# Kernel optimization log

Hardware: AMD Instinct MI355X
Metric: run time of the kernel (lower is better)

Reference implementation:

```python
import jax, jax.numpy as jnp
import numpy as np

NEG_INF = -10000.0


def setup_inputs() -> dict:
    key = jax.random.key(0)
    k_feats, k_mask, k_trans = jax.random.split(key, 3)
    B, S, T = 512, 1024, 64
    feats = jax.random.normal(k_feats, (B, S, T), dtype=jnp.float32)
    masks = jnp.ones((B, S), dtype=jnp.float32)
    # transitions: randn with row 0 and column 0 forced to -10000 (as in __init__)
    transitions = jax.random.normal(k_trans, (T, T), dtype=jnp.float32)
    transitions = transitions.at[:, 0].set(NEG_INF)
    transitions = transitions.at[0, :].set(NEG_INF)
    return {"feats": feats, "masks": masks, "transitions": transitions}


def reference(feats, masks, transitions):
    # feats: [B, S, T], masks: [B, S] float, transitions: [T_next? , T] -> scores
    # scores[b, j, k] = alpha[b, k] + transitions[j, k] + feats[b, i, j]
    # alpha_new[b, j] = logsumexp_k scores[b, j, k]
    alpha0 = feats[:, 0]                      # [B, T]
    feats_t = jnp.swapaxes(feats[:, 1:], 0, 1)   # [S-1, B, T]
    masks_t = masks[:, 1:].T                     # [S-1, B]

    def step(alpha, xm):
        feat_i, mask_i = xm                      # [B, T], [B]
        scores = alpha[:, None, :] + transitions[None] + feat_i[:, :, None]
        new_alpha = jax.scipy.special.logsumexp(scores, axis=2)  # [B, T]
        m = mask_i[:, None]
        alpha = new_alpha * m + alpha * (1.0 - m)
        return alpha, None

    alpha, _ = jax.lax.scan(step, alpha0, (feats_t, masks_t))
    return alpha
```

## Files before the change

kernel.cpp:

```cpp
#include <hip/hip_runtime.h>


typedef _Float16 __attribute__((ext_vector_type(2))) half2v;
typedef _Float16 __attribute__((ext_vector_type(8))) half8v;

constexpr int T    = 64;
constexpr int D    = 6;
constexpr int SMAX = 1024;

__device__ __forceinline__ float fdot2(half2v a, half2v b, float c) {
#if __has_builtin(__builtin_amdgcn_fdot2)
    return __builtin_amdgcn_fdot2(a, b, c, false);
#else
    return fmaf((float)a[0], (float)b[0], fmaf((float)a[1], (float)b[1], c));
#endif
}

__global__ __launch_bounds__(64, 1)
void crf_fwd_kernel(const float* __restrict__ feats,
                    const float* __restrict__ masks,
                    const float* __restrict__ trans,
                    float* __restrict__ out, int S)
{
    const int lane = threadIdx.x;
    const int b    = blockIdx.x;

    __shared__ __attribute__((aligned(16))) _Float16 sh[T];
    __shared__ float shm[SMAX];

    const float* mb = masks + (size_t)b * S;
    for (int w = lane; w < S; w += T) shm[w] = mb[w];

    const float* tr = trans + lane * T;
    float rmax = tr[0];
    for (int j = 1; j < T; ++j) rmax = fmaxf(rmax, tr[j]);
    half2v E[32];
#pragma unroll
    for (int k = 0; k < 32; ++k) {
        E[k][0] = (_Float16)__expf(tr[2 * k]     - rmax);
        E[k][1] = (_Float16)__expf(tr[2 * k + 1] - rmax);
    }

    __syncthreads();

    const float* fb = feats + (size_t)b * S * T;

    const float f0 = fb[lane];
    float u  = __expf(f0);
    _Float16 uh = (_Float16)u;
    float cacc = 0.f;
    float hsnap = 1.f, csnap = 0.f, Rsnap = 0.f, fsnap = f0;

    float f[D], mk[D];
#pragma unroll
    for (int k = 0; k < D; ++k) {
        f[k]  = fb[(size_t)(1 + k) * T + lane];
        mk[k] = shm[1 + k];
    }

#define CRF_STEP(FV, MV)                                                      \
    {                                                                         \
        const float ef = __expf((FV) + rmax);                  \
        const bool  mm = (MV) > 0.5f;                                         \
        __builtin_amdgcn_wave_barrier();                                      \
        sh[lane] = uh;                                                        \
        __builtin_amdgcn_wave_barrier();                                      \
        union { half8v v; half2v h2[4]; } blk[8];                             \
        _Pragma("unroll")                                                     \
        for (int r = 0; r < 8; ++r)                                           \
            blk[r].v = *(const half8v*)(sh + 8 * r);       \
        __builtin_amdgcn_wave_barrier();                                      \
        float ac0 = 0.f, ac1 = 0.f, ac2 = 0.f, ac3 = 0.f;                     \
        float ac4 = 0.f, ac5 = 0.f, ac6 = 0.f, ac7 = 0.f;                     \
        _Pragma("unroll")                                                     \
        for (int r = 0; r < 8; r += 2) {                                      \
            ac0 = fdot2(E[4 * r + 0], blk[r].h2[0], ac0);                     \
            ac1 = fdot2(E[4 * r + 1], blk[r].h2[1], ac1);                     \
            ac2 = fdot2(E[4 * r + 2], blk[r].h2[2], ac2);                     \
            ac3 = fdot2(E[4 * r + 3], blk[r].h2[3], ac3);                     \
            ac4 = fdot2(E[4 * r + 4], blk[r + 1].h2[0], ac4);                 \
            ac5 = fdot2(E[4 * r + 5], blk[r + 1].h2[1], ac5);                 \
            ac6 = fdot2(E[4 * r + 6], blk[r + 1].h2[2], ac6);                 \
            ac7 = fdot2(E[4 * r + 7], blk[r + 1].h2[3], ac7);                 \
        }                                                                     \
        const float total = ((ac0 + ac1) + (ac2 + ac3))                       \
                          + ((ac4 + ac5) + (ac6 + ac7));                      \
                         \
        const int hb = __builtin_amdgcn_readlane(__float_as_int(total), 0);   \
        const int e  = ((hb >> 23) & 255) - 127;                              \
        const float un = ldexpf(ef * total, -e);                              \
        hsnap = mm ? total    : hsnap;                                        \
        csnap = mm ? cacc     : csnap;                \
        Rsnap = mm ? -10000.f : Rsnap;                                        \
        fsnap = mm ? (FV)     : fsnap;                                        \
        u     = mm ? un       : u;                                            \
        cacc  = mm ? fmaf((float)e, 0.69314718055994531f, cacc) : cacc;       \
        uh = (_Float16)u;                                                     \
    }

    int sc = 1;
    for (; sc + D <= S; sc += D) {
#pragma unroll
        for (int k = 0; k < D; ++k) {
            const float fv = f[k];
            const float mv = mk[k];
            const int spre = (sc + k + D < S) ? (sc + k + D) : (S - 1);
            f[k]  = fb[(size_t)spre * T + lane];
            mk[k] = shm[spre];
            CRF_STEP(fv, mv);
        }
    }
#pragma unroll
    for (int k = 0; k < D - 1; ++k) {
        if (sc + k < S) {
            const float fv = f[k];
            const float mv = mk[k];
            CRF_STEP(fv, mv);
        }
    }
#undef CRF_STEP

    float alpha = __logf(u) + cacc;
    if (lane == 0) alpha = fsnap + Rsnap + __logf(hsnap) + csnap;
    out[b * T + lane] = alpha;
}

extern "C" void kernel_launch(void* const* d_in, const int* in_sizes, int n_in,
                              void* d_out, int out_size, void* d_ws, size_t ws_size,
                              hipStream_t stream) {
    const float* feats = (const float*)d_in[0];
    const float* masks = (const float*)d_in[1];
    const float* trans = (const float*)d_in[2];
    float* out = (float*)d_out;

    const int S = 1024;
    const int B = in_sizes[1] / S;
    crf_fwd_kernel<<<B, T, 0, stream>>>(feats, masks, trans, out, S);
}
```

Measured before the change: 385.5 us.

## Process two batch rows per wavefront to interleave independent recurrences

Each 64-thread block now advances two independent CRF forward recurrences (batch rows A and B) in lockstep, sharing the exp-transition registers and interleaving their LDS exchanges, dot products and normalisation. The aim is instruction-level parallelism that hides the latency of the serial per-step dependency chain, while halving the grid to 256 blocks. The prefetch depth drops from 6 to 4 to keep register pressure manageable. The trade-off is fewer wavefronts across the CUs and higher VGPR use per wave.

```diff
diff --git a/kernel.cpp b/kernel.cpp
--- a/kernel.cpp
+++ b/kernel.cpp
@@ -5,7 +5,7 @@
 typedef _Float16 __attribute__((ext_vector_type(8))) half8v;
 
 constexpr int T    = 64;
-constexpr int D    = 6;
+constexpr int D    = 4;
 constexpr int SMAX = 1024;
 
 __device__ __forceinline__ float fdot2(half2v a, half2v b, float c) {
@@ -20,16 +20,24 @@
 void crf_fwd_kernel(const float* __restrict__ feats,
                     const float* __restrict__ masks,
                     const float* __restrict__ trans,
-                    float* __restrict__ out, int S)
+                    float* __restrict__ out, int S, int B)
 {
     const int lane = threadIdx.x;
-    const int b    = blockIdx.x;
+    const int blk  = blockIdx.x;
+    const int bA   = 2 * blk;
+    const int bB   = (2 * blk + 1 < B) ? (2 * blk + 1) : (B - 1);
 
-    __shared__ __attribute__((aligned(16))) _Float16 sh[T];
-    __shared__ float shm[SMAX];
+    __shared__ __attribute__((aligned(16))) _Float16 shA[T];
+    __shared__ __attribute__((aligned(16))) _Float16 shB[T];
+    __shared__ float shmA[SMAX];
+    __shared__ float shmB[SMAX];
 
-    const float* mb = masks + (size_t)b * S;
-    for (int w = lane; w < S; w += T) shm[w] = mb[w];
+    const float* mbA = masks + (size_t)bA * S;
+    const float* mbB = masks + (size_t)bB * S;
+    for (int w = lane; w < S; w += T) {
+        shmA[w] = mbA[w];
+        shmB[w] = mbB[w];
+    }
 
     const float* tr = trans + lane * T;
     float rmax = tr[0];
@@ -43,86 +51,124 @@
 
     __syncthreads();
 
-    const float* fb = feats + (size_t)b * S * T;
+    const float* fbA = feats + (size_t)bA * S * T;
+    const float* fbB = feats + (size_t)bB * S * T;
 
-    const float f0 = fb[lane];
-    float u  = __expf(f0);
-    _Float16 uh = (_Float16)u;
-    float cacc = 0.f;
-    float hsnap = 1.f, csnap = 0.f, Rsnap = 0.f, fsnap = f0;
+    const float f0A = fbA[lane];
+    const float f0B = fbB[lane];
+    float uA = __expf(f0A), uB = __expf(f0B);
+    _Float16 uhA = (_Float16)uA, uhB = (_Float16)uB;
+    float caccA = 0.f, caccB = 0.f;
+    float hsnapA = 1.f, csnapA = 0.f, RsnapA = 0.f, fsnapA = f0A;
+    float hsnapB = 1.f, csnapB = 0.f, RsnapB = 0.f, fsnapB = f0B;
 
-    float f[D], mk[D];
+    float fA[D], mkA[D], fB[D], mkB[D];
 #pragma unroll
     for (int k = 0; k < D; ++k) {
-        f[k]  = fb[(size_t)(1 + k) * T + lane];
-        mk[k] = shm[1 + k];
+        fA[k]  = fbA[(size_t)(1 + k) * T + lane];
+        mkA[k] = shmA[1 + k];
+        fB[k]  = fbB[(size_t)(1 + k) * T + lane];
+        mkB[k] = shmB[1 + k];
     }
 
-#define CRF_STEP(FV, MV)                                                      \
+#define CRF_STEP2(FVA, MVA, FVB, MVB)                                         \
     {                                                                         \
-        const float ef = __expf((FV) + rmax);                  \
-        const bool  mm = (MV) > 0.5f;                                         \
+        const float efA = __expf((FVA) + rmax);                \
+        const float efB = __expf((FVB) + rmax);                               \
+        const bool  mmA = (MVA) > 0.5f;                                       \
+        const bool  mmB = (MVB) > 0.5f;                                       \
         __builtin_amdgcn_wave_barrier();                                      \
-        sh[lane] = uh;                                                        \
+        shA[lane] = uhA;                                                      \
+        shB[lane] = uhB;                                                      \
         __builtin_amdgcn_wave_barrier();                                      \
-        union { half8v v; half2v h2[4]; } blk[8];                             \
+        union { half8v v; half2v h2[4]; } blkA[8], blkB[8];                   \
         _Pragma("unroll")                                                     \
-        for (int r = 0; r < 8; ++r)                                           \
-            blk[r].v = *(const half8v*)(sh + 8 * r);       \
+        for (int r = 0; r < 8; ++r) {                                         \
+            blkA[r].v = *(const half8v*)(shA + 8 * r);     \
+            blkB[r].v = *(const half8v*)(shB + 8 * r);                        \
+        }                                                                     \
         __builtin_amdgcn_wave_barrier();                                      \
-        float ac0 = 0.f, ac1 = 0.f, ac2 = 0.f, ac3 = 0.f;                     \
-        float ac4 = 0.f, ac5 = 0.f, ac6 = 0.f, ac7 = 0.f;                     \
+        float aA0 = 0.f, aA1 = 0.f, aA2 = 0.f, aA3 = 0.f;                     \
+        float aA4 = 0.f, aA5 = 0.f, aA6 = 0.f, aA7 = 0.f;                     \
+        float aB0 = 0.f, aB1 = 0.f, aB2 = 0.f, aB3 = 0.f;                     \
+        float aB4 = 0.f, aB5 = 0.f, aB6 = 0.f, aB7 = 0.f;                     \
         _Pragma("unroll")                                                     \
         for (int r = 0; r < 8; r += 2) {                                      \
-            ac0 = fdot2(E[4 * r + 0], blk[r].h2[0], ac0);                     \
-            ac1 = fdot2(E[4 * r + 1], blk[r].h2[1], ac1);                     \
-            ac2 = fdot2(E[4 * r + 2], blk[r].h2[2], ac2);                     \
-            ac3 = fdot2(E[4 * r + 3], blk[r].h2[3], ac3);                     \
-            ac4 = fdot2(E[4 * r + 4], blk[r + 1].h2[0], ac4);                 \
-            ac5 = fdot2(E[4 * r + 5], blk[r + 1].h2[1], ac5);                 \
-            ac6 = fdot2(E[4 * r + 6], blk[r + 1].h2[2], ac6);                 \
-            ac7 = fdot2(E[4 * r + 7], blk[r + 1].h2[3], ac7);                 \
+            aA0 = fdot2(E[4 * r + 0], blkA[r].h2[0], aA0);                    \
+            aA1 = fdot2(E[4 * r + 1], blkA[r].h2[1], aA1);                    \
+            aA2 = fdot2(E[4 * r + 2], blkA[r].h2[2], aA2);                    \
+            aA3 = fdot2(E[4 * r + 3], blkA[r].h2[3], aA3);                    \
+            aA4 = fdot2(E[4 * r + 4], blkA[r + 1].h2[0], aA4);                \
+            aA5 = fdot2(E[4 * r + 5], blkA[r + 1].h2[1], aA5);                \
+            aA6 = fdot2(E[4 * r + 6], blkA[r + 1].h2[2], aA6);                \
+            aA7 = fdot2(E[4 * r + 7], blkA[r + 1].h2[3], aA7);                \
+            aB0 = fdot2(E[4 * r + 0], blkB[r].h2[0], aB0);                    \
+            aB1 = fdot2(E[4 * r + 1], blkB[r].h2[1], aB1);                    \
+            aB2 = fdot2(E[4 * r + 2], blkB[r].h2[2], aB2);                    \
+            aB3 = fdot2(E[4 * r + 3], blkB[r].h2[3], aB3);                    \
+            aB4 = fdot2(E[4 * r + 4], blkB[r + 1].h2[0], aB4);                \
+            aB5 = fdot2(E[4 * r + 5], blkB[r + 1].h2[1], aB5);                \
+            aB6 = fdot2(E[4 * r + 6], blkB[r + 1].h2[2], aB6);                \
+            aB7 = fdot2(E[4 * r + 7], blkB[r + 1].h2[3], aB7);                \
         }                                                                     \
-        const float total = ((ac0 + ac1) + (ac2 + ac3))                       \
-                          + ((ac4 + ac5) + (ac6 + ac7));                      \
-                         \
-        const int hb = __builtin_amdgcn_readlane(__float_as_int(total), 0);   \
-        const int e  = ((hb >> 23) & 255) - 127;                              \
-        const float un = ldexpf(ef * total, -e);                              \
-        hsnap = mm ? total    : hsnap;                                        \
-        csnap = mm ? cacc     : csnap;                \
-        Rsnap = mm ? -10000.f : Rsnap;                                        \
-        fsnap = mm ? (FV)     : fsnap;                                        \
-        u     = mm ? un       : u;                                            \
-        cacc  = mm ? fmaf((float)e, 0.69314718055994531f, cacc) : cacc;       \
-        uh = (_Float16)u;                                                     \
+        const float totalA = ((aA0 + aA1) + (aA2 + aA3))                      \
+                           + ((aA4 + aA5) + (aA6 + aA7));                     \
+        const float totalB = ((aB0 + aB1) + (aB2 + aB3))                      \
+                           + ((aB4 + aB5) + (aB6 + aB7));                     \
+        const int hbA = __builtin_amdgcn_readlane(__float_as_int(totalA), 0); \
+        const int hbB = __builtin_amdgcn_readlane(__float_as_int(totalB), 0); \
+        const int eA  = ((hbA >> 23) & 255) - 127;                            \
+        const int eB  = ((hbB >> 23) & 255) - 127;                            \
+        const float unA = ldexpf(efA * totalA, -eA);                          \
+        const float unB = ldexpf(efB * totalB, -eB);                          \
+        hsnapA = mmA ? totalA   : hsnapA;                                     \
+        csnapA = mmA ? caccA    : csnapA;                                     \
+        RsnapA = mmA ? -10000.f : RsnapA;                                     \
+        fsnapA = mmA ? (FVA)    : fsnapA;                                     \
+        uA     = mmA ? unA      : uA;                                         \
+        caccA  = mmA ? fmaf((float)eA, 0.69314718055994531f, caccA) : caccA;  \
+        hsnapB = mmB ? totalB   : hsnapB;                                     \
+        csnapB = mmB ? caccB    : csnapB;                                     \
+        RsnapB = mmB ? -10000.f : RsnapB;                                     \
+        fsnapB = mmB ? (FVB)    : fsnapB;                                     \
+        uB     = mmB ? unB      : uB;                                         \
+        caccB  = mmB ? fmaf((float)eB, 0.69314718055994531f, caccB) : caccB;  \
+        uhA = (_Float16)uA;                                                   \
+        uhB = (_Float16)uB;                                                   \
     }
 
     int sc = 1;
     for (; sc + D <= S; sc += D) {
 #pragma unroll
         for (int k = 0; k < D; ++k) {
-            const float fv = f[k];
-            const float mv = mk[k];
+            const float fvA = fA[k], mvA = mkA[k];
+            const float fvB = fB[k], mvB = mkB[k];
             const int spre = (sc + k + D < S) ? (sc + k + D) : (S - 1);
-            f[k]  = fb[(size_t)spre * T + lane];
-            mk[k] = shm[spre];
-            CRF_STEP(fv, mv);
+            fA[k]  = fbA[(size_t)spre * T + lane];
+            mkA[k] = shmA[spre];
+            fB[k]  = fbB[(size_t)spre * T + lane];
+            mkB[k] = shmB[spre];
+            CRF_STEP2(fvA, mvA, fvB, mvB);
         }
     }
 #pragma unroll
     for (int k = 0; k < D - 1; ++k) {
         if (sc + k < S) {
-            const float fv = f[k];
-            const float mv = mk[k];
-            CRF_STEP(fv, mv);
+            const float fvA = fA[k], mvA = mkA[k];
+            const float fvB = fB[k], mvB = mkB[k];
+            CRF_STEP2(fvA, mvA, fvB, mvB);
         }
     }
-#undef CRF_STEP
+#undef CRF_STEP2
 
-    float alpha = __logf(u) + cacc;
-    if (lane == 0) alpha = fsnap + Rsnap + __logf(hsnap) + csnap;
-    out[b * T + lane] = alpha;
+    float alphaA = __logf(uA) + caccA;
+    float alphaB = __logf(uB) + caccB;
+    if (lane == 0) {
+        alphaA = fsnapA + RsnapA + __logf(hsnapA) + csnapA;
+        alphaB = fsnapB + RsnapB + __logf(hsnapB) + csnapB;
+    }
+    out[(size_t)bA * T + lane] = alphaA;
+    out[(size_t)bB * T + lane] = alphaB;
 }
 
 extern "C" void kernel_launch(void* const* d_in, const int* in_sizes, int n_in,
@@ -135,5 +181,6 @@
 
     const int S = 1024;
     const int B = in_sizes[1] / S;
-    crf_fwd_kernel<<<B, T, 0, stream>>>(feats, masks, trans, out, S);
+    const int grid = (B + 1) / 2;
+    crf_fwd_kernel<<<grid, T, 0, stream>>>(feats, masks, trans, out, S, B);
 }
```

Result: slower. 608.3 us (+57.8%).

## Replace LDS broadcast of alpha with cross-lane DPP/permlane allgather

Applied to the files above, without the earlier changes.

Each step used to write the fp16 alpha value to shared memory and read it back as 64 halves per lane. It now gathers all 64 values across the wave in registers using DPP, v_perm and v_permlane swap instructions. The transition-matrix operands are permuted to match the order the gather produces. The goal is to take LDS latency and wave barriers off the serial recurrence, at the cost of more VALU/DPP instructions per step and hazard nops.

```diff
diff --git a/kernel.cpp b/kernel.cpp
--- a/kernel.cpp
+++ b/kernel.cpp
@@ -1,8 +1,8 @@
 #include <hip/hip_runtime.h>
+#include <stdint.h>
 
 
 typedef _Float16 __attribute__((ext_vector_type(2))) half2v;
-typedef _Float16 __attribute__((ext_vector_type(8))) half8v;
 
 constexpr int T    = 64;
 constexpr int D    = 6;
@@ -16,6 +16,43 @@
 #endif
 }
 
+__device__ __forceinline__ half2v as_h2(uint32_t x) {
+    union { uint32_t u; half2v h; } c; c.u = x; return c.h;
+}
+
+#define DPPM(SRC, CTRL)                                                       \
+    ((uint32_t)__builtin_amdgcn_update_dpp(0, (int)(SRC), (CTRL), 0xF, 0xF, false))
+
+
+__device__ __forceinline__ void allgather64(uint32_t c, uint32_t O[32]) {
+    uint32_t n1 = DPPM(c, 0xB1);
+    uint32_t p0 = __builtin_amdgcn_perm(n1, c, 0x05040100u);
+    uint32_t q0 = p0, q1;
+    asm("v_mov_b32 %1, %0\n\t"
+        "s_nop 1\n\t"
+        "v_permlane32_swap_b32 %0, %1"
+        : "+v"(q0), "=&v"(q1));
+    uint32_t r0 = q0, r1, r2 = q1, r3;
+    asm("v_mov_b32 %1, %0\n\t"
+        "s_nop 1\n\t"
+        "v_permlane16_swap_b32 %0, %1"
+        : "+v"(r0), "=&v"(r1));
+    asm("v_mov_b32 %1, %0\n\t"
+        "s_nop 1\n\t"
+        "v_permlane16_swap_b32 %0, %1"
+        : "+v"(r2), "=&v"(r3));
+    uint32_t t[16];
+    t[0] = r0; t[1] = r1; t[2] = r2; t[3] = r3;
+#pragma unroll
+    for (int i = 0; i < 4; ++i) t[4 + i] = DPPM(t[i], 0x4E);
+#pragma unroll
+    for (int i = 0; i < 8; ++i) t[8 + i] = DPPM(t[i], 0x124);
+#pragma unroll
+    for (int i = 0; i < 16; ++i) O[i] = t[i];
+#pragma unroll
+    for (int i = 0; i < 16; ++i) O[16 + i] = DPPM(t[i], 0x128);
+}
+
 __global__ __launch_bounds__(64, 1)
 void crf_fwd_kernel(const float* __restrict__ feats,
                     const float* __restrict__ masks,
@@ -25,7 +62,6 @@
     const int lane = threadIdx.x;
     const int b    = blockIdx.x;
 
-    __shared__ __attribute__((aligned(16))) _Float16 sh[T];
     __shared__ float shm[SMAX];
 
     const float* mb = masks + (size_t)b * S;
@@ -34,11 +70,16 @@
     const float* tr = trans + lane * T;
     float rmax = tr[0];
     for (int j = 1; j < T; ++j) rmax = fmaxf(rmax, tr[j]);
+
+    uint32_t idx[32];
+    allgather64((uint32_t)lane, idx);
     half2v E[32];
 #pragma unroll
     for (int k = 0; k < 32; ++k) {
-        E[k][0] = (_Float16)__expf(tr[2 * k]     - rmax);
-        E[k][1] = (_Float16)__expf(tr[2 * k + 1] - rmax);
+        const int j0 = (int)(idx[k] & 0xffffu);
+        const int j1 = (int)(idx[k] >> 16);
+        E[k][0] = (_Float16)__expf(tr[j0] - rmax);
+        E[k][1] = (_Float16)__expf(tr[j1] - rmax);
     }
 
     __syncthreads();
@@ -47,45 +88,38 @@
 
     const float f0 = fb[lane];
     float u  = __expf(f0);
-    _Float16 uh = (_Float16)u;
     float cacc = 0.f;
     float hsnap = 1.f, csnap = 0.f, Rsnap = 0.f, fsnap = f0;
 
-    float f[D], mk[D];
+    float f[D];
 #pragma unroll
-    for (int k = 0; k < D; ++k) {
-        f[k]  = fb[(size_t)(1 + k) * T + lane];
-        mk[k] = shm[1 + k];
+    for (int k = 0; k < D; ++k) f[k] = fb[(size_t)(1 + k) * T + lane];
+    float mcur = shm[1];
+
+    uint32_t O[32];
+    {
+        union { _Float16 h; uint16_t u16; } cv; cv.h = (_Float16)u;
+        allgather64(cv.u16, O);
     }
 
-#define CRF_STEP(FV, MV)                                                      \
+#define CRF_STEP(FV, SNXT)                                                    \
     {                                                                         \
         const float ef = __expf((FV) + rmax);                  \
-        const bool  mm = (MV) > 0.5f;                                         \
-        __builtin_amdgcn_wave_barrier();                                      \
-        sh[lane] = uh;                                                        \
-        __builtin_amdgcn_wave_barrier();                                      \
-        union { half8v v; half2v h2[4]; } blk[8];                             \
+        const bool  mm = mcur > 0.5f;                                         \
+        float a0=0.f,a1=0.f,a2=0.f,a3=0.f,a4=0.f,a5=0.f,a6=0.f,a7=0.f;        \
         _Pragma("unroll")                                                     \
-        for (int r = 0; r < 8; ++r)                                           \
-            blk[r].v = *(const half8v*)(sh + 8 * r);       \
-        __builtin_amdgcn_wave_barrier();                                      \
-        float ac0 = 0.f, ac1 = 0.f, ac2 = 0.f, ac3 = 0.f;                     \
-        float ac4 = 0.f, ac5 = 0.f, ac6 = 0.f, ac7 = 0.f;                     \
-        _Pragma("unroll")                                                     \
-        for (int r = 0; r < 8; r += 2) {                                      \
-            ac0 = fdot2(E[4 * r + 0], blk[r].h2[0], ac0);                     \
-            ac1 = fdot2(E[4 * r + 1], blk[r].h2[1], ac1);                     \
-            ac2 = fdot2(E[4 * r + 2], blk[r].h2[2], ac2);                     \
-            ac3 = fdot2(E[4 * r + 3], blk[r].h2[3], ac3);                     \
-            ac4 = fdot2(E[4 * r + 4], blk[r + 1].h2[0], ac4);                 \
-            ac5 = fdot2(E[4 * r + 5], blk[r + 1].h2[1], ac5);                 \
-            ac6 = fdot2(E[4 * r + 6], blk[r + 1].h2[2], ac6);                 \
-            ac7 = fdot2(E[4 * r + 7], blk[r + 1].h2[3], ac7);                 \
+        for (int t4 = 0; t4 < 4; ++t4) {                                      \
+            a0 = fdot2(E[t4],      as_h2(O[t4]),      a0);                    \
+            a1 = fdot2(E[4 + t4],  as_h2(O[4 + t4]),  a1);                    \
+            a2 = fdot2(E[8 + t4],  as_h2(O[8 + t4]),  a2);                    \
+            a3 = fdot2(E[12 + t4], as_h2(O[12 + t4]), a3);                    \
+            a4 = fdot2(E[16 + t4], as_h2(O[16 + t4]), a4);                    \
+            a5 = fdot2(E[20 + t4], as_h2(O[20 + t4]), a5);                    \
+            a6 = fdot2(E[24 + t4], as_h2(O[24 + t4]), a6);                    \
+            a7 = fdot2(E[28 + t4], as_h2(O[28 + t4]), a7);                    \
         }                                                                     \
-        const float total = ((ac0 + ac1) + (ac2 + ac3))                       \
-                          + ((ac4 + ac5) + (ac6 + ac7));                      \
-                         \
+        const float total = ((a0+a1)+(a2+a3)) + ((a4+a5)+(a6+a7));            \
+             \
         const int hb = __builtin_amdgcn_readlane(__float_as_int(total), 0);   \
         const int e  = ((hb >> 23) & 255) - 127;                              \
         const float un = ldexpf(ef * total, -e);                              \
@@ -95,34 +129,37 @@
         fsnap = mm ? (FV)     : fsnap;                                        \
         u     = mm ? un       : u;                                            \
         cacc  = mm ? fmaf((float)e, 0.69314718055994531f, cacc) : cacc;       \
-        uh = (_Float16)u;                                                     \
+        union { _Float16 h; uint16_t u16; } cv_; cv_.h = (_Float16)u;         \
+        allgather64(cv_.u16, O);                     \
+        mcur = shm[(SNXT)];                     \
     }
 
     int sc = 1;
     for (; sc + D <= S; sc += D) {
 #pragma unroll
         for (int k = 0; k < D; ++k) {
+            const int s    = sc + k;
+            const int spre = (s + D < S) ? (s + D) : (S - 1);
+            const int snxt = (s + 1 < S) ? (s + 1) : (S - 1);
             const float fv = f[k];
-            const float mv = mk[k];
-            const int spre = (sc + k + D < S) ? (sc + k + D) : (S - 1);
-            f[k]  = fb[(size_t)spre * T + lane];
-            mk[k] = shm[spre];
-            CRF_STEP(fv, mv);
+            f[k] = fb[(size_t)spre * T + lane];
+            CRF_STEP(fv, snxt);
         }
     }
 #pragma unroll
     for (int k = 0; k < D - 1; ++k) {
-        if (sc + k < S) {
+        const int s = sc + k;
+        if (s < S) {
+            const int snxt = (s + 1 < S) ? (s + 1) : (S - 1);
             const float fv = f[k];
-            const float mv = mk[k];
-            CRF_STEP(fv, mv);
+            CRF_STEP(fv, snxt);
         }
     }
 #undef CRF_STEP
 
     float alpha = __logf(u) + cacc;
     if (lane == 0) alpha = fsnap + Rsnap + __logf(hsnap) + csnap;
-    out[b * T + lane] = alpha;
+    out[(size_t)b * T + lane] = alpha;
 }
 
 extern "C" void kernel_launch(void* const* d_in, const int* in_sizes, int n_in,
```

Result: slower. 443.7 us (+15.1%).
